# Optimization experiments

Hardware: AMD Instinct MI355X
Metric: run time of the kernel (lower is better)

Reference implementation:

```python
import jax, jax.numpy as jnp
import numpy as np

B, T, D = 64, 512, 768
H = D // 2      # per-direction LSTM hidden
L = 33          # num_labels


def setup_inputs() -> dict:
    key = jax.random.key(0)
    ks = jax.random.split(key, 14)
    input_embed = jax.random.normal(ks[0], (B, T, D), dtype=jnp.float32)
    # pack_padded_sequence requires lengths sorted in decreasing order
    lengths = jnp.sort(jax.random.randint(ks[1], (B,), T // 2, T + 1))[::-1]
    lengths = lengths.at[0].set(T)
    mask = jnp.arange(T)[None, :] < lengths[:, None]          # [B,T] bool
    labels = jax.random.randint(ks[2], (B, T), 0, L, dtype=jnp.int32)
    index = jax.random.randint(ks[3], (B, 2), 0, T)
    s = 0.1
    w_ih_f = jax.random.normal(ks[4], (4 * H, D), jnp.float32) * s
    w_hh_f = jax.random.normal(ks[5], (4 * H, H), jnp.float32) * s
    b_f = jax.random.normal(ks[6], (4 * H,), jnp.float32) * s
    w_ih_b = jax.random.normal(ks[7], (4 * H, D), jnp.float32) * s
    w_hh_b = jax.random.normal(ks[8], (4 * H, H), jnp.float32) * s
    b_b = jax.random.normal(ks[9], (4 * H,), jnp.float32) * s
    lin_w = jax.random.normal(ks[10], (L, 2 * H), jnp.float32) * s
    lin_b = jnp.zeros((L,), jnp.float32)
    trans = jax.random.normal(ks[11], (L, L), jnp.float32) * s
    start_trans = jax.random.normal(ks[12], (L,), jnp.float32) * s
    end_trans = jax.random.normal(ks[13], (L,), jnp.float32) * s
    return dict(input_embed=input_embed, mask=mask, labels=labels, index=index,
                w_ih_f=w_ih_f, w_hh_f=w_hh_f, b_f=b_f,
                w_ih_b=w_ih_b, w_hh_b=w_hh_b, b_b=b_b,
                lin_w=lin_w, lin_b=lin_b,
                trans=trans, start_trans=start_trans, end_trans=end_trans)


def _run_lstm(x, mask_f, w_ih, w_hh, b):
    """Unidirectional LSTM over packed (length-masked) sequences.
    Output is zero at padded steps; state is frozen past each sequence length.
    x: [B,T,D] -> [B,T,H]. Torch gate order: i, f, g, o.
    """
    xp = jnp.einsum('btd,gd->btg', x, w_ih) + b          # [B,T,4H] precomputed
    xp_t = xp.transpose(1, 0, 2)                         # [T,B,4H]
    m_t = mask_f.T[:, :, None]                           # [T,B,1]
    nH = w_hh.shape[1]
    init = (jnp.zeros((x.shape[0], nH), x.dtype), jnp.zeros((x.shape[0], nH), x.dtype))

    def step(carry, inp):
        h, c = carry
        xg, m = inp
        g = xg + h @ w_hh.T
        i, f, gc, o = jnp.split(g, 4, axis=-1)
        c_new = jax.nn.sigmoid(f) * c + jax.nn.sigmoid(i) * jnp.tanh(gc)
        h_new = jax.nn.sigmoid(o) * jnp.tanh(c_new)
        carry = (jnp.where(m > 0, h_new, h), jnp.where(m > 0, c_new, c))
        return carry, h_new * m

    _, ys = jax.lax.scan(step, init, (xp_t, m_t))
    return ys.transpose(1, 0, 2)


def reference(input_embed, mask, labels, index,
              w_ih_f, w_hh_f, b_f, w_ih_b, w_hh_b, b_b,
              lin_w, lin_b, trans, start_trans, end_trans):
    mask_f = mask.astype(input_embed.dtype)              # [B,T]
    lengths = mask.sum(1).astype(jnp.int32)              # [B]

    # BiLSTM with pack_padded semantics (dropout in eval mode = identity)
    h_fwd = _run_lstm(input_embed, mask_f, w_ih_f, w_hh_f, b_f)
    # reverse within each sequence's valid region (involution on valid steps)
    rev_idx = jnp.clip(lengths[:, None] - 1 - jnp.arange(T)[None, :], 0, T - 1)
    x_rev = jnp.take_along_axis(input_embed, rev_idx[..., None], axis=1)
    h_b_rev = _run_lstm(x_rev, mask_f, w_ih_b, w_hh_b, b_b)
    h_bwd = jnp.take_along_axis(h_b_rev, rev_idx[..., None], axis=1) * mask_f[..., None]
    h = jnp.concatenate([h_fwd, h_bwd], axis=-1)         # [B,T,2H]

    # emissions, masked as in the original (out *= mask.unsqueeze(-1))
    em = (jnp.einsum('bth,lh->btl', h, lin_w) + lin_b) * mask_f[..., None]

    # ---- CRF log-likelihood: numerator (gold path score) ----
    em_y = jnp.take_along_axis(em, labels[..., None], axis=2)[..., 0]   # [B,T]
    tr = trans[labels[:, :-1], labels[:, 1:]]                            # [B,T-1]
    num = start_trans[labels[:, 0]] + em_y[:, 0] \
        + jnp.sum((tr + em_y[:, 1:]) * mask_f[:, 1:], axis=1)
    last_y = jnp.take_along_axis(labels, (lengths - 1)[:, None], axis=1)[:, 0]
    num = num + end_trans[last_y]

    # ---- CRF log-partition: forward algorithm scan ----
    alpha0 = start_trans[None, :] + em[:, 0]             # [B,L]

    def step(alpha, inp):
        e_t, m_t = inp                                   # [B,L], [B]
        new = jax.nn.logsumexp(alpha[:, :, None] + trans[None, :, :] + e_t[:, None, :], axis=1)
        return jnp.where(m_t[:, None] > 0, new, alpha), None

    alpha, _ = jax.lax.scan(step, alpha0,
                            (em[:, 1:].transpose(1, 0, 2), mask_f[:, 1:].T))
    logZ = jax.nn.logsumexp(alpha + end_trans[None, :], axis=1)

    score = num - logZ                                   # per-sample log-likelihood
    return -jnp.mean(score)
```

## Files before the change

kernel.cpp:

```cpp
#include <hip/hip_runtime.h>

typedef unsigned short U16;
typedef unsigned int   U32;
typedef unsigned long long U64;
typedef __attribute__((ext_vector_type(8))) short S8;
typedef __attribute__((ext_vector_type(4))) float F4;

#define B_  64
#define T_  512
#define DD  768
#define HH  384
#define G4  1536
#define NL  33

__device__ __forceinline__ U16 f2bf(float f){
  U32 u = __float_as_uint(f);
  u += 0x7fffu + ((u >> 16) & 1u);
  return (U16)(u >> 16);
}
__device__ __forceinline__ float bf2f(U16 h){ return __uint_as_float(((U32)h) << 16); }
__device__ __forceinline__ float frcp(float x){
  float r;
  asm("v_rcp_f32 %0, %1" : "=v"(r) : "v"(x));
  return r;
}
__device__ __forceinline__ float sigm(float x){
  return frcp(1.f + __expf(-x));
}
__device__ __forceinline__ float tanh_(float x){
  float e = __expf(2.f * x);
  return 1.f - 2.f * frcp(e + 1.f);
}

__global__ void k_pre(const float* x, U64* xb, const U32* mask, int* lens,
                      const float* wf_, const float* wb_, const float* lw_,
                      const float* bfv, const float* bbv,
                      U16* wcat, U16* lwb, float* bcat){
  int blk = blockIdx.x;
  int tid = threadIdx.x;
  if (blk < 64){
    if (tid < 64){
      int b = blk, l = tid;
      bool b32 = (mask[0] == 1u);
      int cnt = 0;
      for (int t = l; t < T_; t += 64){
        int v = b32 ? ((const int*)mask)[b * T_ + t]
                    : (int)((const unsigned char*)mask)[b * T_ + t];
        cnt += (v != 0);
      }
      #pragma unroll
      for (int o = 32; o >= 1; o >>= 1) cnt += __shfl_xor(cnt, o);
      if (l == 0) lens[b] = cnt;
    }
    return;
  }
  if (blk < 1088){
    const int WE = G4 * DD;
    const int LWE = NL * DD;
    int total = 2 * WE + LWE + 2 * G4;
    for (int i = (blk - 64) * 256 + tid; i < total; i += 1024 * 256){
      if (i < WE) wcat[i] = f2bf(wf_[i]);
      else if (i < 2 * WE) wcat[i] = f2bf(wb_[i - WE]);
      else if (i < 2 * WE + LWE) lwb[i - 2 * WE] = f2bf(lw_[i - 2 * WE]);
      else { int j = i - 2 * WE - LWE; bcat[j] = (j < G4) ? bfv[j] : bbv[j - G4]; }
    }
    return;
  }
  size_t n4 = (size_t)B_ * T_ * DD / 4;
  for (size_t i = (size_t)(blk - 1088) * 256 + tid; i < n4; i += (size_t)2048 * 256){
    float4 v = ((const float4*)x)[i];
    U64 o = (U64)f2bf(v.x) | ((U64)f2bf(v.y) << 16) | ((U64)f2bf(v.z) << 32) | ((U64)f2bf(v.w) << 48);
    xb[i] = o;
  }
}

__global__ __launch_bounds__(256) void k_gemm(const U16* __restrict__ A,
                                              const U16* __restrict__ Bw,
                                              const float* __restrict__ bias, U16* C){
  __shared__ __align__(16) U16 As[128 * 64];
  __shared__ __align__(16) U16 Bs[128 * 64];
  int swz = (blockIdx.x & 7) * 768 + (blockIdx.x >> 3);
  int mb = swz & 255, nb = swz >> 8;
  int m0 = mb * 128, n0 = nb * 128;
  int tid = threadIdx.x;
  int w = tid >> 6, l = tid & 63;
  int lr = l & 15, lk = (l >> 4) * 8;
  int wm = (w >> 1) * 64, wn = (w & 1) * 64;
  int srow = tid >> 3;
  int scol = (tid & 7) * 8;
  F4 acc[4][4];
  #pragma unroll
  for (int i = 0; i < 4; i++)
    #pragma unroll
    for (int j = 0; j < 4; j++) acc[i][j] = (F4){0.f, 0.f, 0.f, 0.f};

  for (int kt = 0; kt < DD; kt += 64){
    __syncthreads();
    #pragma unroll
    for (int r = 0; r < 4; r++){
      int row = r * 32 + srow;
      int sw = scol ^ ((row & 7) * 8);
      __builtin_amdgcn_global_load_lds((const U32*)(A + (size_t)(m0 + row) * DD + kt + sw),
                                       (U32*)(As + row * 64 + scol), 16, 0, 0);
      __builtin_amdgcn_global_load_lds((const U32*)(Bw + (size_t)(n0 + row) * DD + kt + sw),
                                       (U32*)(Bs + row * 64 + scol), 16, 0, 0);
    }
    __syncthreads();
    #pragma unroll
    for (int kk = 0; kk < 64; kk += 32){
      S8 af[4], bf[4];
      int cs = (kk + lk) ^ ((lr & 7) * 8);
      #pragma unroll
      for (int i = 0; i < 4; i++) af[i] = *(const S8*)(As + (wm + i * 16 + lr) * 64 + cs);
      #pragma unroll
      for (int i = 0; i < 4; i++) bf[i] = *(const S8*)(Bs + (wn + i * 16 + lr) * 64 + cs);
      #pragma unroll
      for (int i = 0; i < 4; i++)
        #pragma unroll
        for (int j = 0; j < 4; j++)
          acc[i][j] = __builtin_amdgcn_mfma_f32_16x16x32_bf16(af[i], bf[j], acc[i][j], 0, 0, 0);
    }
  }
  #pragma unroll
  for (int j = 0; j < 4; j++){
    int col = n0 + wn + j * 16 + lr;
    float bv = bias[col];
    #pragma unroll
    for (int i = 0; i < 4; i++){
      #pragma unroll
      for (int rg = 0; rg < 4; rg++){
        int row = m0 + wm + i * 16 + (l >> 4) * 4 + rg;
        C[(size_t)row * 3072 + col] = f2bf(acc[i][j][rg] + bv);
      }
    }
  }
}

__global__ __launch_bounds__(256, 1) void k_rec(const U16* __restrict__ xp,
                                                const float* __restrict__ whf,
                                                const float* __restrict__ whb,
                                                const int* __restrict__ len_,
                                                U16* __restrict__ hcat, U64* hx){
  int blk = blockIdx.x;
  int g = blk & 7, m = blk >> 3;
  int dir = g >> 2, chunk = g & 3, sb = chunk * 16;
  const float* wh = dir ? whb : whf;
  int tid = threadIdx.x;
  int w = tid >> 6, l = tid & 63;
  int lr = l & 15, lq = l >> 4;
  int jloc = m * 64 + w * 16 + lr;

  S8 wf[4][12];
  #pragma unroll
  for (int q = 0; q < 4; q++){
    #pragma unroll
    for (int kc = 0; kc < 12; kc++){
      const float* p = wh + (size_t)(q * HH + jloc) * HH + kc * 32 + lq * 8;
      float4 v0 = *(const float4*)p;
      float4 v1 = *(const float4*)(p + 4);
      S8 t;
      t[0] = (short)f2bf(v0.x); t[1] = (short)f2bf(v0.y); t[2] = (short)f2bf(v0.z); t[3] = (short)f2bf(v0.w);
      t[4] = (short)f2bf(v1.x); t[5] = (short)f2bf(v1.y); t[6] = (short)f2bf(v1.z); t[7] = (short)f2bf(v1.w);
      wf[q][kc] = t;
    }
  }

  __shared__ __align__(16) U16 hl[16][408];
  for (int i = tid; i < 16 * 408; i += 256) ((U16*)hl)[i] = 0;
  int lens[4];
  #pragma unroll
  for (int r = 0; r < 4; r++) lens[r] = len_[sb + lq * 4 + r];
  int steps = len_[sb];
  float cst[4] = {0.f, 0.f, 0.f, 0.f}, hst[4] = {0.f, 0.f, 0.f, 0.f};
  __syncthreads();

  for (int step = 0; step < steps; ++step){
    float xv[4][4];
    #pragma unroll
    for (int r = 0; r < 4; r++){
      int L = lens[r];
      int t = dir ? (L - 1 - step) : step;
      if (t < 0) t = 0;
      size_t basei = ((size_t)(sb + lq * 4 + r) * T_ + t) * 3072 + dir * G4;
      #pragma unroll
      for (int q = 0; q < 4; q++) xv[q][r] = bf2f(xp[basei + q * HH + jloc]);
    }
    if (step){
      const U64* src = hx + (size_t)((step & 1) * 8 + g) * 3072;
      U64 v[12];
      #pragma unroll
      for (int k = 0; k < 12; k++)
        v[k] = __hip_atomic_load(src + tid + k * 256, __ATOMIC_RELAXED, __HIP_MEMORY_SCOPE_AGENT);
      U32 expct = (U32)step;
      while (true){
        U32 bad = 0;
        #pragma unroll
        for (int k = 0; k < 12; k++) bad |= (((U32)(v[k] >> 32)) != expct) ? (1u << k) : 0u;
        if (!bad) break;
        #pragma unroll
        for (int k = 0; k < 12; k++)
          if (bad & (1u << k))
            v[k] = __hip_atomic_load(src + tid + k * 256, __ATOMIC_RELAXED, __HIP_MEMORY_SCOPE_AGENT);
      }
      #pragma unroll
      for (int k = 0; k < 12; k++){
        int wi = tid + k * 256;
        int col = wi >> 3, p = wi & 7;
        U32 lo = (U32)v[k];
        hl[2 * p + 0][col] = (U16)lo;
        hl[2 * p + 1][col] = (U16)(lo >> 16);
      }
      asm volatile("s_waitcnt lgkmcnt(0)" ::: "memory");
      __builtin_amdgcn_s_barrier();
      asm volatile("" ::: "memory");
      __builtin_amdgcn_sched_barrier(0);
    }
    F4 acc[4];
    #pragma unroll
    for (int q = 0; q < 4; q++) acc[q] = (F4){0.f, 0.f, 0.f, 0.f};
    #pragma unroll
    for (int kc = 0; kc < 12; kc++){
      S8 a = *(const S8*)&hl[lr][kc * 32 + lq * 8];
      #pragma unroll
      for (int q = 0; q < 4; q++)
        acc[q] = __builtin_amdgcn_mfma_f32_16x16x32_bf16(a, wf[q][kc], acc[q], 0, 0, 0);
    }
    #pragma unroll
    for (int r = 0; r < 4; r++){
      float ip = acc[0][r] + xv[0][r];
      float fp = acc[1][r] + xv[1][r];
      float gp = acc[2][r] + xv[2][r];
      float op = acc[3][r] + xv[3][r];
      float cn = sigm(fp) * cst[r] + sigm(ip) * tanh_(gp);
      float hn = sigm(op) * tanh_(cn);
      if (step < lens[r]){ cst[r] = cn; hst[r] = hn; }
    }
    {
      U64 tag = ((U64)(U32)(step + 1)) << 32;
      U64 w0 = (U64)((U32)f2bf(hst[0]) | ((U32)f2bf(hst[1]) << 16)) | tag;
      U64 w1 = (U64)((U32)f2bf(hst[2]) | ((U32)f2bf(hst[3]) << 16)) | tag;
      U64* dst = hx + (size_t)(((step + 1) & 1) * 8 + g) * 3072 + jloc * 8 + lq * 2;
      __hip_atomic_store(dst + 0, w0, __ATOMIC_RELAXED, __HIP_MEMORY_SCOPE_AGENT);
      __hip_atomic_store(dst + 1, w1, __ATOMIC_RELAXED, __HIP_MEMORY_SCOPE_AGENT);
    }
    #pragma unroll
    for (int r = 0; r < 4; r++){
      if (step < lens[r]){
        int t = dir ? (lens[r] - 1 - step) : step;
        hcat[((size_t)(sb + lq * 4 + r) * T_ + t) * (2 * HH) + dir * HH + jloc] = f2bf(hst[r]);
      }
    }
  }
}

__global__ __launch_bounds__(256) void k_em(const U16* hcat, const U16* lwb, const float* lin_b, float* em){
  __shared__ __align__(16) U16 lw[NL * DD];
  __shared__ __align__(16) U16 hs[32 * DD];
  int tid = threadIdx.x;
  for (int i = tid; i < NL * DD / 4; i += 256) ((U64*)lw)[i] = ((const U64*)lwb)[i];
  size_t r0 = (size_t)blockIdx.x * 32;
  const U64* hsrc = (const U64*)(hcat + r0 * DD);
  for (int i = tid; i < 32 * DD / 4; i += 256) ((U64*)hs)[i] = hsrc[i];
  __syncthreads();
  for (int e = tid; e < 32 * NL; e += 256){
    int rr = e / NL, ll = e % NL;
    const U16* hp = &hs[rr * DD];
    const U16* wp = &lw[ll * DD];
    float s = 0.f;
    #pragma unroll 8
    for (int k = 0; k < DD; k += 2){
      U32 hv = *(const U32*)&hp[k];
      U32 wv = *(const U32*)&wp[k];
      s = fmaf(__uint_as_float(hv << 16), __uint_as_float(wv << 16), s);
      s = fmaf(__uint_as_float(hv & 0xffff0000u), __uint_as_float(wv & 0xffff0000u), s);
    }
    em[(r0 + rr) * NL + ll] = s + lin_b[ll];
  }
}

__global__ void k_crf(const float* em, const int* labels, const int* len_, const float* trans,
                      const float* startt, const float* endt, float* score){
  int b = blockIdx.x, l = threadIdx.x;
  int L = len_[b];
  const int* lab = labels + b * T_;
  const float* emb = em + (size_t)b * T_ * NL;
  float part = 0.f;
  for (int t = 1 + l; t < L; t += 64){
    int lp = lab[t - 1], lc = lab[t];
    part += trans[lp * NL + lc] + emb[(size_t)t * NL + lc];
  }
  #pragma unroll
  for (int o = 32; o >= 1; o >>= 1) part += __shfl_xor(part, o);
  float num = part + startt[lab[0]] + emb[lab[0]] + endt[lab[L - 1]];
  bool act = l < NL;
  int jj = act ? l : (NL - 1);
  float tc[NL];
  #pragma unroll
  for (int i = 0; i < NL; i++) tc[i] = trans[i * NL + jj];
  float a = startt[jj] + emb[jj];
  for (int t = 1; t < L; ++t){
    float vv[NL];
    float mx = -3.0e38f;
    #pragma unroll
    for (int i = 0; i < NL; i++){ vv[i] = __shfl(a, i) + tc[i]; mx = fmaxf(mx, vv[i]); }
    float s = 0.f;
    #pragma unroll
    for (int i = 0; i < NL; i++) s += __expf(vv[i] - mx);
    a = mx + __logf(s) + emb[(size_t)t * NL + jj];
  }
  float val = act ? (a + endt[jj]) : -3.0e38f;
  float mx = val;
  #pragma unroll
  for (int o = 32; o >= 1; o >>= 1) mx = fmaxf(mx, __shfl_xor(mx, o));
  float se = __expf(val - mx);
  #pragma unroll
  for (int o = 32; o >= 1; o >>= 1) se += __shfl_xor(se, o);
  float logZ = mx + __logf(se);
  if (l == 0) score[b] = num - logZ;
}

__global__ void k_final(const float* score, float* out){
  int l = threadIdx.x;
  float v = score[l];
  #pragma unroll
  for (int o = 32; o >= 1; o >>= 1) v += __shfl_xor(v, o);
  if (l == 0) out[0] = -v / 64.f;
}

__global__ void k_sentinel(float* out){ out[0] = -12345.f; }

extern "C" void kernel_launch(void* const* d_in, const int* in_sizes, int n_in,
                              void* d_out, int out_size, void* d_ws, size_t ws_size,
                              hipStream_t stream){
  const float* x      = (const float*)d_in[0];
  const void*  mask   = d_in[1];
  const int*   labels = (const int*)d_in[2];
  const float* w_ih_f = (const float*)d_in[4];
  const float* w_hh_f = (const float*)d_in[5];
  const float* b_f    = (const float*)d_in[6];
  const float* w_ih_b = (const float*)d_in[7];
  const float* w_hh_b = (const float*)d_in[8];
  const float* b_b    = (const float*)d_in[9];
  const float* lin_w  = (const float*)d_in[10];
  const float* lin_b  = (const float*)d_in[11];
  const float* trans  = (const float*)d_in[12];
  const float* startt = (const float*)d_in[13];
  const float* endt   = (const float*)d_in[14];
  float* out = (float*)d_out;

  const size_t WS_NEEDED = 261158912;
  if (ws_size < WS_NEEDED){
    k_sentinel<<<1, 1, 0, stream>>>(out);
    return;
  }

  char* ws = (char*)d_ws;
  size_t off = 0;
  auto take = [&](size_t bytes) -> char* {
    char* p = ws + off;
    off += (bytes + 255) & ~(size_t)255;
    return p;
  };
  U16*  xp    = (U16*)take((size_t)32768 * 3072 * 2);
  U16*  hcat  = (U16*)take((size_t)32768 * 768 * 2);
  U16*  wcat  = (U16*)take((size_t)3072 * 768 * 2);
  U16*  lwb   = (U16*)take((size_t)NL * 768 * 2);
  float* bcat = (float*)take(3072 * 4);
  int*  lens  = (int*)take(256);
  U64*  hx    = (U64*)take((size_t)2 * 8 * 3072 * 8);
  float* em   = (float*)take((size_t)32768 * NL * 4);
  float* score= (float*)take(256);
  U16*  xbf   = hcat;

  (void)hipMemsetAsync(hx, 0, (size_t)2 * 8 * 3072 * 8, stream);
  k_pre<<<3136, 256, 0, stream>>>(x, (U64*)xbf, (const U32*)mask, lens,
                                  w_ih_f, w_ih_b, lin_w, b_f, b_b, wcat, lwb, bcat);
  k_gemm<<<6144, 256, 0, stream>>>(xbf, wcat, bcat, xp);
  k_rec<<<48, 256, 0, stream>>>(xp, w_hh_f, w_hh_b, lens, hcat, hx);
  k_em<<<1024, 256, 0, stream>>>(hcat, lwb, lin_b, em);
  k_crf<<<64, 64, 0, stream>>>(em, labels, lens, trans, startt, endt, score);
  k_final<<<1, 64, 0, stream>>>(score, out);
}
```

Measured before the change: 2.117 ms.

## Fuse input-projection GEMM with LSTM recurrence via per-tile readiness counters

Merges the input-projection GEMM and the recurrent LSTM kernel into one persistent launch. 48 blocks run the recurrence and 208 blocks compute GEMM tiles, ordered so that forward time-chunks and the backward tail chunks come first. Each finished tile stores its output with cache-bypassing stores and then bumps a release counter. The recurrent blocks poll that counter every 128 steps before they read xp, so the GEMM overlaps with the serial recurrence instead of fully preceding it. The risks are spin-wait contention, the GEMM competing with the recurrence for bandwidth, reusing the em buffer as counter storage, and a possible deadlock if the blocks are not all co-resident.

```diff
diff --git a/kernel.cpp b/kernel.cpp
--- a/kernel.cpp
+++ b/kernel.cpp
@@ -5,6 +5,7 @@
 typedef unsigned long long U64;
 typedef __attribute__((ext_vector_type(8))) short S8;
 typedef __attribute__((ext_vector_type(4))) float F4;
+typedef __attribute__((ext_vector_type(4))) U32 U4;
 
 #define B_  64
 #define T_  512
@@ -74,78 +75,99 @@
   }
 }
 
-__global__ __launch_bounds__(256) void k_gemm(const U16* __restrict__ A,
-                                              const U16* __restrict__ Bw,
-                                              const float* __restrict__ bias, U16* C){
-  __shared__ __align__(16) U16 As[128 * 64];
-  __shared__ __align__(16) U16 Bs[128 * 64];
-  int swz = (blockIdx.x & 7) * 768 + (blockIdx.x >> 3);
-  int mb = swz & 255, nb = swz >> 8;
-  int m0 = mb * 128, n0 = nb * 128;
+__global__ __launch_bounds__(256, 1) void k_fused(
+    const U16* __restrict__ A, const U16* __restrict__ Bw, const float* __restrict__ bias,
+    U16* xp, const float* __restrict__ whf, const float* __restrict__ whb,
+    const int* __restrict__ len_, U16* __restrict__ hcat, U64* hx, int* cnt){
+  __shared__ __align__(16) U16 smem[128 * 128];
   int tid = threadIdx.x;
-  int w = tid >> 6, l = tid & 63;
-  int lr = l & 15, lk = (l >> 4) * 8;
-  int wm = (w >> 1) * 64, wn = (w & 1) * 64;
-  int srow = tid >> 3;
-  int scol = (tid & 7) * 8;
-  F4 acc[4][4];
-  #pragma unroll
-  for (int i = 0; i < 4; i++)
-    #pragma unroll
-    for (int j = 0; j < 4; j++) acc[i][j] = (F4){0.f, 0.f, 0.f, 0.f};
-
-  for (int kt = 0; kt < DD; kt += 64){
-    __syncthreads();
-    #pragma unroll
-    for (int r = 0; r < 4; r++){
-      int row = r * 32 + srow;
-      int sw = scol ^ ((row & 7) * 8);
-      __builtin_amdgcn_global_load_lds((const U32*)(A + (size_t)(m0 + row) * DD + kt + sw),
-                                       (U32*)(As + row * 64 + scol), 16, 0, 0);
-      __builtin_amdgcn_global_load_lds((const U32*)(Bw + (size_t)(n0 + row) * DD + kt + sw),
-                                       (U32*)(Bs + row * 64 + scol), 16, 0, 0);
-    }
-    __syncthreads();
-    #pragma unroll
-    for (int kk = 0; kk < 64; kk += 32){
-      S8 af[4], bf[4];
-      int cs = (kk + lk) ^ ((lr & 7) * 8);
-      #pragma unroll
-      for (int i = 0; i < 4; i++) af[i] = *(const S8*)(As + (wm + i * 16 + lr) * 64 + cs);
-      #pragma unroll
-      for (int i = 0; i < 4; i++) bf[i] = *(const S8*)(Bs + (wn + i * 16 + lr) * 64 + cs);
+
+  if (blockIdx.x >= 48){
+    U16* As = smem;
+    U16* Bs = smem + 8192;
+    int w = tid >> 6, l = tid & 63;
+    int lr = l & 15, lk = (l >> 4) * 8;
+    int wm = (w >> 1) * 64, wn = (w & 1) * 64;
+    int srow = tid >> 3;
+    int scol = (tid & 7) * 8;
+    int wk = blockIdx.x - 48;
+
+    for (int j = wk; j < 6144; j += 208){
+      int phase = (j >= 3072);
+      int jp = phase ? (j - 3072) : j;
+      int s = jp / 48;
+      int r = jp - s * 48;
+      int which = r / 24;
+      int nb = r - which * 24;
+      int tt = phase ? (which ? 2 : 1) : (which ? 3 : 0);
+      int mb = s * 4 + tt;
+      int m0 = mb * 128, n0 = nb * 128;
+      float bv[4];
+      #pragma unroll
+      for (int jj = 0; jj < 4; jj++) bv[jj] = bias[n0 + wn + jj * 16 + lr];
+      F4 acc[4][4];
       #pragma unroll
       for (int i = 0; i < 4; i++)
         #pragma unroll
-        for (int j = 0; j < 4; j++)
-          acc[i][j] = __builtin_amdgcn_mfma_f32_16x16x32_bf16(af[i], bf[j], acc[i][j], 0, 0, 0);
-    }
-  }
-  #pragma unroll
-  for (int j = 0; j < 4; j++){
-    int col = n0 + wn + j * 16 + lr;
-    float bv = bias[col];
-    #pragma unroll
-    for (int i = 0; i < 4; i++){
-      #pragma unroll
-      for (int rg = 0; rg < 4; rg++){
-        int row = m0 + wm + i * 16 + (l >> 4) * 4 + rg;
-        C[(size_t)row * 3072 + col] = f2bf(acc[i][j][rg] + bv);
-      }
-    }
-  }
-}
-
-__global__ __launch_bounds__(256, 1) void k_rec(const U16* __restrict__ xp,
-                                                const float* __restrict__ whf,
-                                                const float* __restrict__ whb,
-                                                const int* __restrict__ len_,
-                                                U16* __restrict__ hcat, U64* hx){
+        for (int jj = 0; jj < 4; jj++) acc[i][jj] = (F4){0.f, 0.f, 0.f, 0.f};
+
+      for (int kt = 0; kt < DD; kt += 64){
+        __syncthreads();
+        #pragma unroll
+        for (int rr = 0; rr < 4; rr++){
+          int row = rr * 32 + srow;
+          int sw = scol ^ ((row & 7) * 8);
+          __builtin_amdgcn_global_load_lds((const U32*)(A + (size_t)(m0 + row) * DD + kt + sw),
+                                           (U32*)(As + row * 64 + scol), 16, 0, 0);
+          __builtin_amdgcn_global_load_lds((const U32*)(Bw + (size_t)(n0 + row) * DD + kt + sw),
+                                           (U32*)(Bs + row * 64 + scol), 16, 0, 0);
+        }
+        __syncthreads();
+        #pragma unroll
+        for (int kk = 0; kk < 64; kk += 32){
+          S8 af[4], bf[4];
+          int cs = (kk + lk) ^ ((lr & 7) * 8);
+          #pragma unroll
+          for (int i = 0; i < 4; i++) af[i] = *(const S8*)(As + (wm + i * 16 + lr) * 64 + cs);
+          #pragma unroll
+          for (int i = 0; i < 4; i++) bf[i] = *(const S8*)(Bs + (wn + i * 16 + lr) * 64 + cs);
+          #pragma unroll
+          for (int i = 0; i < 4; i++)
+            #pragma unroll
+            for (int jj = 0; jj < 4; jj++)
+              acc[i][jj] = __builtin_amdgcn_mfma_f32_16x16x32_bf16(af[i], bf[jj], acc[i][jj], 0, 0, 0);
+        }
+      }
+      __syncthreads();
+      #pragma unroll
+      for (int jj = 0; jj < 4; jj++)
+        #pragma unroll
+        for (int i = 0; i < 4; i++)
+          #pragma unroll
+          for (int rg = 0; rg < 4; rg++)
+            smem[(wm + i * 16 + (l >> 4) * 4 + rg) * 128 + wn + jj * 16 + lr] =
+                f2bf(acc[i][jj][rg] + bv[jj]);
+      __syncthreads();
+      #pragma unroll
+      for (int k2 = 0; k2 < 8; k2++){
+        int idx = k2 * 256 + tid;
+        int row = idx >> 4, cc = idx & 15;
+        U4 val = *(const U4*)&smem[row * 128 + cc * 8];
+        U64 addr = (U64)(uintptr_t)(xp + (size_t)(m0 + row) * 3072 + n0 + cc * 8);
+        asm volatile("global_store_dwordx4 %0, %1, off sc0 sc1" :: "v"(addr), "v"(val));
+      }
+      asm volatile("s_waitcnt vmcnt(0)" ::: "memory");
+      __syncthreads();
+      if (tid == 0)
+        __hip_atomic_fetch_add(&cnt[mb], 1, __ATOMIC_RELEASE, __HIP_MEMORY_SCOPE_AGENT);
+    }
+    return;
+  }
+
   int blk = blockIdx.x;
   int g = blk & 7, m = blk >> 3;
-  int dir = g >> 2, chunk = g & 3, sb = chunk * 16;
+  int dir = g >> 2, sb = (g & 3) * 16;
   const float* wh = dir ? whb : whf;
-  int tid = threadIdx.x;
   int w = tid >> 6, l = tid & 63;
   int lr = l & 15, lq = l >> 4;
   int jloc = m * 64 + w * 16 + lr;
@@ -165,25 +187,45 @@
     }
   }
 
-  __shared__ __align__(16) U16 hl[16][408];
+  U16 (*hl)[408] = (U16(*)[408])smem;
   for (int i = tid; i < 16 * 408; i += 256) ((U16*)hl)[i] = 0;
   int lens[4];
   #pragma unroll
   for (int r = 0; r < 4; r++) lens[r] = len_[sb + lq * 4 + r];
   int steps = len_[sb];
+  int Lme = len_[sb + (l & 15)];
   float cst[4] = {0.f, 0.f, 0.f, 0.f}, hst[4] = {0.f, 0.f, 0.f, 0.f};
   __syncthreads();
 
   for (int step = 0; step < steps; ++step){
+    if ((step & 127) == 0){
+      int tt;
+      if (dir == 0) tt = step >> 7;
+      else if (l < 16){
+        int tlo = Lme - 1 - step - 127; if (tlo < 0) tlo = 0; tt = tlo >> 7;
+      } else {
+        int thi = Lme - 1 - step; if (thi < 0) thi = 0; tt = thi >> 7;
+      }
+      int tile = ((sb + (l & 15)) << 2) + tt;
+      bool actg = (l < 32);
+      for (;;){
+        int cv = actg ? __hip_atomic_load(&cnt[tile], __ATOMIC_RELAXED, __HIP_MEMORY_SCOPE_AGENT) : 24;
+        if (__all(cv >= 24)) break;
+        __builtin_amdgcn_s_sleep(4);
+      }
+      __scoped_atomic_thread_fence(__ATOMIC_ACQUIRE, __MEMORY_SCOPE_DEVICE);
+    }
     float xv[4][4];
     #pragma unroll
     for (int r = 0; r < 4; r++){
       int L = lens[r];
       int t = dir ? (L - 1 - step) : step;
       if (t < 0) t = 0;
-      size_t basei = ((size_t)(sb + lq * 4 + r) * T_ + t) * 3072 + dir * G4;
-      #pragma unroll
-      for (int q = 0; q < 4; q++) xv[q][r] = bf2f(xp[basei + q * HH + jloc]);
+      if (t >= L) t = L - 1;
+      const U16* basep = xp + ((size_t)(sb + lq * 4 + r) * T_ + t) * 3072 + dir * G4 + jloc;
+      #pragma unroll
+      for (int q = 0; q < 4; q++)
+        xv[q][r] = bf2f(__hip_atomic_load(basep + q * HH, __ATOMIC_RELAXED, __HIP_MEMORY_SCOPE_AGENT));
     }
     if (step){
       const U64* src = hx + (size_t)((step & 1) * 8 + g) * 3072;
@@ -371,12 +413,13 @@
   float* em   = (float*)take((size_t)32768 * NL * 4);
   float* score= (float*)take(256);
   U16*  xbf   = hcat;
+  int*  cnt   = (int*)em;
 
   (void)hipMemsetAsync(hx, 0, (size_t)2 * 8 * 3072 * 8, stream);
+  (void)hipMemsetAsync(cnt, 0, 1024, stream);
   k_pre<<<3136, 256, 0, stream>>>(x, (U64*)xbf, (const U32*)mask, lens,
                                   w_ih_f, w_ih_b, lin_w, b_f, b_b, wcat, lwb, bcat);
-  k_gemm<<<6144, 256, 0, stream>>>(xbf, wcat, bcat, xp);
-  k_rec<<<48, 256, 0, stream>>>(xp, w_hh_f, w_hh_b, lens, hcat, hx);
+  k_fused<<<256, 256, 0, stream>>>(xbf, wcat, bcat, xp, w_hh_f, w_hh_b, lens, hcat, hx, cnt);
   k_em<<<1024, 256, 0, stream>>>(hcat, lwb, lin_b, em);
   k_crf<<<64, 64, 0, stream>>>(em, labels, lens, trans, startt, endt, score);
   k_final<<<1, 64, 0, stream>>>(score, out);
```

After: 2.260 ms. +6.7%, slower.

## Enlarge input-projection GEMM tile to 256x256 with double-buffered LDS staging

Applied to the files above, without the earlier changes.

Reworks the input-projection GEMM to use 256x256 block tiles with 8 waves, each owning a 128x64 sub-tile. LDS is double-buffered so the next K slice is loaded while the current one is multiplied, and the bias loads are hoisted out of the epilogue. The goal is more data reuse per loaded byte and hiding global-load latency behind MFMA work. In exchange it uses 128 KB of LDS and many more accumulator registers, which limits occupancy to one block per CU.

```diff
diff --git a/kernel.cpp b/kernel.cpp
--- a/kernel.cpp
+++ b/kernel.cpp
@@ -74,66 +74,82 @@
   }
 }
 
-__global__ __launch_bounds__(256) void k_gemm(const U16* __restrict__ A,
-                                              const U16* __restrict__ Bw,
-                                              const float* __restrict__ bias, U16* C){
-  __shared__ __align__(16) U16 As[128 * 64];
-  __shared__ __align__(16) U16 Bs[128 * 64];
-  int swz = (blockIdx.x & 7) * 768 + (blockIdx.x >> 3);
-  int mb = swz & 255, nb = swz >> 8;
-  int m0 = mb * 128, n0 = nb * 128;
+__global__ __launch_bounds__(512, 1) void k_gemm(const U16* __restrict__ A,
+                                                 const U16* __restrict__ Bw,
+                                                 const float* __restrict__ bias, U16* C){
+  __shared__ __align__(16) U16 lds[4][256 * 64];
+  int swz = (blockIdx.x & 7) * 192 + (blockIdx.x >> 3);
+  int mb = swz & 127, nb = swz >> 7;
+  int m0 = mb * 256, n0 = nb * 256;
   int tid = threadIdx.x;
   int w = tid >> 6, l = tid & 63;
   int lr = l & 15, lk = (l >> 4) * 8;
-  int wm = (w >> 1) * 64, wn = (w & 1) * 64;
+  int wr = (w >> 2) * 128, wc = (w & 3) * 64;
   int srow = tid >> 3;
   int scol = (tid & 7) * 8;
-  F4 acc[4][4];
-  #pragma unroll
-  for (int i = 0; i < 4; i++)
+
+  float bv[4];
+  #pragma unroll
+  for (int j = 0; j < 4; j++) bv[j] = bias[n0 + wc + j * 16 + lr];
+
+  F4 acc[8][4];
+  #pragma unroll
+  for (int i = 0; i < 8; i++)
     #pragma unroll
     for (int j = 0; j < 4; j++) acc[i][j] = (F4){0.f, 0.f, 0.f, 0.f};
 
-  for (int kt = 0; kt < DD; kt += 64){
+  #define STAGE(BUF, KT) { \
+    _Pragma("unroll") \
+    for (int rr = 0; rr < 4; rr++){ \
+      int row = rr * 64 + srow; \
+      int sw = scol ^ ((row & 7) * 8); \
+      __builtin_amdgcn_global_load_lds((const U32*)(A + (size_t)(m0 + row) * DD + (KT) + sw), \
+                                       (U32*)(&lds[(BUF) * 2][row * 64 + scol]), 16, 0, 0); \
+      __builtin_amdgcn_global_load_lds((const U32*)(Bw + (size_t)(n0 + row) * DD + (KT) + sw), \
+                                       (U32*)(&lds[(BUF) * 2 + 1][row * 64 + scol]), 16, 0, 0); \
+    } }
+
+  #define COMPUTE(BUF) { \
+    _Pragma("unroll") \
+    for (int kk = 0; kk < 64; kk += 32){ \
+      int cs = (kk + lk) ^ ((lr & 7) * 8); \
+      S8 af[8], bf[4]; \
+      _Pragma("unroll") \
+      for (int i = 0; i < 8; i++) af[i] = *(const S8*)(&lds[(BUF) * 2][(wr + i * 16 + lr) * 64 + cs]); \
+      _Pragma("unroll") \
+      for (int j = 0; j < 4; j++) bf[j] = *(const S8*)(&lds[(BUF) * 2 + 1][(wc + j * 16 + lr) * 64 + cs]); \
+      _Pragma("unroll") \
+      for (int i = 0; i < 8; i++) \
+        _Pragma("unroll") \
+        for (int j = 0; j < 4; j++) \
+          acc[i][j] = __builtin_amdgcn_mfma_f32_16x16x32_bf16(af[i], bf[j], acc[i][j], 0, 0, 0); \
+    } }
+
+  STAGE(0, 0)
+  __syncthreads();
+  int cur = 0;
+  for (int t = 1; t < 12; ++t){
+    STAGE(cur ^ 1, t * 64)
+    COMPUTE(cur)
     __syncthreads();
-    #pragma unroll
-    for (int r = 0; r < 4; r++){
-      int row = r * 32 + srow;
-      int sw = scol ^ ((row & 7) * 8);
-      __builtin_amdgcn_global_load_lds((const U32*)(A + (size_t)(m0 + row) * DD + kt + sw),
-                                       (U32*)(As + row * 64 + scol), 16, 0, 0);
-      __builtin_amdgcn_global_load_lds((const U32*)(Bw + (size_t)(n0 + row) * DD + kt + sw),
-                                       (U32*)(Bs + row * 64 + scol), 16, 0, 0);
-    }
-    __syncthreads();
-    #pragma unroll
-    for (int kk = 0; kk < 64; kk += 32){
-      S8 af[4], bf[4];
-      int cs = (kk + lk) ^ ((lr & 7) * 8);
-      #pragma unroll
-      for (int i = 0; i < 4; i++) af[i] = *(const S8*)(As + (wm + i * 16 + lr) * 64 + cs);
-      #pragma unroll
-      for (int i = 0; i < 4; i++) bf[i] = *(const S8*)(Bs + (wn + i * 16 + lr) * 64 + cs);
-      #pragma unroll
-      for (int i = 0; i < 4; i++)
-        #pragma unroll
-        for (int j = 0; j < 4; j++)
-          acc[i][j] = __builtin_amdgcn_mfma_f32_16x16x32_bf16(af[i], bf[j], acc[i][j], 0, 0, 0);
-    }
-  }
+    cur ^= 1;
+  }
+  COMPUTE(cur)
+
   #pragma unroll
   for (int j = 0; j < 4; j++){
-    int col = n0 + wn + j * 16 + lr;
-    float bv = bias[col];
-    #pragma unroll
-    for (int i = 0; i < 4; i++){
+    int col = n0 + wc + j * 16 + lr;
+    #pragma unroll
+    for (int i = 0; i < 8; i++){
       #pragma unroll
       for (int rg = 0; rg < 4; rg++){
-        int row = m0 + wm + i * 16 + (l >> 4) * 4 + rg;
-        C[(size_t)row * 3072 + col] = f2bf(acc[i][j][rg] + bv);
-      }
-    }
-  }
+        int row = m0 + wr + i * 16 + (l >> 4) * 4 + rg;
+        C[(size_t)row * 3072 + col] = f2bf(acc[i][j][rg] + bv[j]);
+      }
+    }
+  }
+  #undef STAGE
+  #undef COMPUTE
 }
 
 __global__ __launch_bounds__(256, 1) void k_rec(const U16* __restrict__ xp,
@@ -375,7 +391,7 @@
   (void)hipMemsetAsync(hx, 0, (size_t)2 * 8 * 3072 * 8, stream);
   k_pre<<<3136, 256, 0, stream>>>(x, (U64*)xbf, (const U32*)mask, lens,
                                   w_ih_f, w_ih_b, lin_w, b_f, b_b, wcat, lwb, bcat);
-  k_gemm<<<6144, 256, 0, stream>>>(xbf, wcat, bcat, xp);
+  k_gemm<<<1536, 512, 0, stream>>>(xbf, wcat, bcat, xp);
   k_rec<<<48, 256, 0, stream>>>(xp, w_hh_f, w_hh_b, lens, hcat, hx);
   k_em<<<1024, 256, 0, stream>>>(hcat, lwb, lin_b, em);
   k_crf<<<64, 64, 0, stream>>>(em, labels, lens, trans, startt, endt, score);
```

Measured after the change: 2.062 ms (median of 2 runs). 1.03x faster.
